# Performance work log

Measured on AMD Instinct MI355X. Metric: run time of the kernel, lower is better.

The kernel has to match this reference:

```python
import jax, jax.numpy as jnp
import numpy as np

B, C, H, W = 8, 21, 512, 512
MAX_M = 0.5   # args.ldam_max_m
S = 30.0      # args.ldam_s


def setup_inputs() -> dict:
    key = jax.random.key(0)
    k1, k2 = jax.random.split(key)
    pred = jax.random.normal(k1, (B, C, H, W), dtype=jnp.float32)
    target = jax.random.randint(k2, (B, H, W), 0, C, dtype=jnp.int32)  # class labels (argmax of one-hot)
    return {"pred": pred, "target": target}


def reference(pred, target):
    labels = target.reshape(-1)  # [N]
    # m_list: per-class pixel counts == sum of one-hot target over (0,2,3)
    counts = jnp.zeros((C,), dtype=pred.dtype).at[labels].add(1.0)
    m_list = 1.0 / jnp.sqrt(jnp.sqrt(counts + 1e-4))
    m_list = m_list * (MAX_M / jnp.max(m_list))

    logits = pred.transpose(0, 2, 3, 1).reshape(-1, C)  # [N, C]
    batch_m = m_list[labels]                            # gather == matmul(m_list, one_hot^T)
    onehot = jax.nn.one_hot(labels, C, dtype=logits.dtype)
    output = logits - batch_m[:, None] * onehot         # subtract margin only at target class

    logp = jax.nn.log_softmax(S * output, axis=-1)
    nll = -jnp.take_along_axis(logp, labels[:, None].astype(jnp.int32), axis=1)[:, 0]
    return jnp.mean(nll)
```

## Files before the change

kernel.cpp:

```cpp
#include <hip/hip_runtime.h>

static constexpr int   Cc  = 21;
static constexpr int   HWn = 512 * 512;
static constexpr int   Nn  = 8 * HWn;
static constexpr float MAXM  = 0.5f;
static constexpr float Sc    = 30.0f;
static constexpr float LOG2E = 1.4426950408889634f;
static constexpr float LN2   = 0.6931471805599453f;

static constexpr int WS_COUNTS = 0;
static constexpr int WS_ACC    = 96;
static constexpr int WS_SM     = 128;

__global__ __launch_bounds__(256) void hist_kernel(const int4* __restrict__ t4,
                                                   int* __restrict__ counts) {
    __shared__ int lh[Cc];
    int t = threadIdx.x;
    if (t < Cc) lh[t] = 0;
    __syncthreads();
    int tid = blockIdx.x * 256 + t;
    int4 v = t4[tid];
    atomicAdd(&lh[v.x], 1);
    atomicAdd(&lh[v.y], 1);
    atomicAdd(&lh[v.z], 1);
    atomicAdd(&lh[v.w], 1);
    __syncthreads();
    if (t < Cc) atomicAdd(&counts[t], lh[t]);
}

__global__ __launch_bounds__(64) void mlist_kernel(const int* __restrict__ counts,
                                                   float* __restrict__ sm2) {
    int t = threadIdx.x;
    float mval = 0.0f;
    if (t < Cc) {
        float cnt = (float)counts[t] + 1e-4f;
        mval = 1.0f / sqrtf(sqrtf(cnt));
    }
    float mx = mval;
    #pragma unroll
    for (int o = 32; o >= 1; o >>= 1) mx = fmaxf(mx, __shfl_down(mx, o));
    mx = __shfl(mx, 0);
    if (t < Cc) sm2[t] = Sc * LOG2E * mval * (MAXM / mx);
}

__global__ __launch_bounds__(256, 2) void loss_kernel(const float* __restrict__ pred,
                                                      const int4* __restrict__ t4,
                                                      const float* __restrict__ smg,
                                                      double* __restrict__ acc) {
    __shared__ float s_sm[Cc];
    __shared__ float wsum[4];
    int t = threadIdx.x;
    if (t < Cc) s_sm[t] = smg[t];
    __syncthreads();

    int tid = blockIdx.x * 256 + t;
    int n0  = tid * 4;
    int b   = n0 >> 18;
    int hw  = n0 & (HWn - 1);
    const float4* p4 = (const float4*)(pred + (size_t)b * Cc * HWn + hw);

    float4 x[Cc];
    #pragma unroll
    for (int c = 0; c < Cc; ++c) x[c] = p4[(size_t)c * (HWn / 4)];

    int4 y4 = t4[tid];
    int ys[4] = {y4.x, y4.y, y4.z, y4.w};
    float smy[4];
    #pragma unroll
    for (int k = 0; k < 4; ++k) smy[k] = s_sm[ys[k]];

    const float S2 = Sc * LOG2E;

    float mx[4] = {-1e30f, -1e30f, -1e30f, -1e30f};
    float vy[4] = {0.f, 0.f, 0.f, 0.f};
    #pragma unroll
    for (int c = 0; c < Cc; ++c) {
        float xs[4] = {x[c].x, x[c].y, x[c].z, x[c].w};
        #pragma unroll
        for (int k = 0; k < 4; ++k) {
            bool  isy = (c == ys[k]);
            float val = fmaf(S2, xs[k], isy ? -smy[k] : 0.0f);
            mx[k] = fmaxf(mx[k], val);
            vy[k] = isy ? val : vy[k];
        }
    }

    float nll2 = 0.0f;
    #pragma unroll
    for (int k = 0; k < 4; ++k) {
        float cb = -mx[k];
        float cy = -smy[k] - mx[k];
        float sum = 0.0f;
        #pragma unroll
        for (int c = 0; c < Cc; ++c) {
            float xs = (k == 0) ? x[c].x : (k == 1) ? x[c].y : (k == 2) ? x[c].z : x[c].w;
            sum += exp2f(fmaf(S2, xs, (c == ys[k]) ? cy : cb));
        }
        nll2 += __log2f(sum) + mx[k] - vy[k];
    }
    float nll = nll2 * LN2;

    #pragma unroll
    for (int o = 32; o >= 1; o >>= 1) nll += __shfl_down(nll, o);

    int wave = t >> 6;
    int lane = t & 63;
    if (lane == 0) wsum[wave] = nll;
    __syncthreads();
    if (t == 0) {
        float bsum = wsum[0] + wsum[1] + wsum[2] + wsum[3];
        atomicAdd(acc, (double)bsum);
    }
}

__global__ void final_kernel(const double* __restrict__ acc, float* __restrict__ out) {
    out[0] = (float)(acc[0] / (double)Nn);
}

extern "C" void kernel_launch(void* const* d_in, const int* in_sizes, int n_in,
                              void* d_out, int out_size, void* d_ws, size_t ws_size,
                              hipStream_t stream) {
    const float* pred   = (const float*)d_in[0];
    const int*   target = (const int*)d_in[1];
    float*       out    = (float*)d_out;

    char* ws = (char*)d_ws;
    int*    counts = (int*)(ws + WS_COUNTS);
    double* acc    = (double*)(ws + WS_ACC);
    float*  sm     = (float*)(ws + WS_SM);

    hipMemsetAsync(d_ws, 0, 256, stream);

    hist_kernel <<<Nn / 4 / 256, 256, 0, stream>>>((const int4*)target, counts);
    mlist_kernel<<<1,            64,  0, stream>>>(counts, sm);
    loss_kernel <<<Nn / 4 / 256, 256, 0, stream>>>(pred, (const int4*)target, sm, acc);
    final_kernel<<<1,            1,   0, stream>>>(acc, out);
}
```

Measured before the change: 272.4 us.

## Fold mlist and final kernels into last-block epilogues; halve hist blocks

Removes the single-block mlist and final kernels by having the last finishing block of the histogram kernel compute the margin list, and the last block of the loss kernel write the mean, using atomic done counters with thread fences. The histogram kernel now processes two int4 per thread with per-wave shared-memory sub-histograms to cut LDS atomic contention and halve the block count. This saves two kernel launches and their gaps, at the cost of extra global atomics and fences at the end of each block.

```diff
diff --git a/kernel.cpp b/kernel.cpp
--- a/kernel.cpp
+++ b/kernel.cpp
@@ -8,45 +8,66 @@
 static constexpr float LOG2E = 1.4426950408889634f;
 static constexpr float LN2   = 0.6931471805599453f;
 
-static constexpr int WS_COUNTS = 0;
-static constexpr int WS_ACC    = 96;
-static constexpr int WS_SM     = 128;
+static constexpr int WS_COUNTS    = 0;
+static constexpr int WS_HIST_DONE = 88;
+static constexpr int WS_LOSS_DONE = 92;
+static constexpr int WS_ACC       = 96;
+static constexpr int WS_SM        = 112;
 
 __global__ __launch_bounds__(256) void hist_kernel(const int4* __restrict__ t4,
-                                                   int* __restrict__ counts) {
-    __shared__ int lh[Cc];
-    int t = threadIdx.x;
-    if (t < Cc) lh[t] = 0;
+                                                   int* __restrict__ counts,
+                                                   int* __restrict__ hist_done,
+                                                   float* __restrict__ sm2) {
+    __shared__ int lh[4][Cc];
+    __shared__ int is_last;
+    int t    = threadIdx.x;
+    int wave = t >> 6;
+    if (t < Cc) { lh[0][t] = 0; lh[1][t] = 0; lh[2][t] = 0; lh[3][t] = 0; }
     __syncthreads();
+
     int tid = blockIdx.x * 256 + t;
-    int4 v = t4[tid];
-    atomicAdd(&lh[v.x], 1);
-    atomicAdd(&lh[v.y], 1);
-    atomicAdd(&lh[v.z], 1);
-    atomicAdd(&lh[v.w], 1);
+    int4 a = t4[tid];
+    int4 b = t4[tid + (Nn / 8)];
+    atomicAdd(&lh[wave][a.x], 1);
+    atomicAdd(&lh[wave][a.y], 1);
+    atomicAdd(&lh[wave][a.z], 1);
+    atomicAdd(&lh[wave][a.w], 1);
+    atomicAdd(&lh[wave][b.x], 1);
+    atomicAdd(&lh[wave][b.y], 1);
+    atomicAdd(&lh[wave][b.z], 1);
+    atomicAdd(&lh[wave][b.w], 1);
     __syncthreads();
-    if (t < Cc) atomicAdd(&counts[t], lh[t]);
-}
+    if (t < Cc) atomicAdd(&counts[t], lh[0][t] + lh[1][t] + lh[2][t] + lh[3][t]);
+    __syncthreads();
 
-__global__ __launch_bounds__(64) void mlist_kernel(const int* __restrict__ counts,
-                                                   float* __restrict__ sm2) {
-    int t = threadIdx.x;
-    float mval = 0.0f;
-    if (t < Cc) {
-        float cnt = (float)counts[t] + 1e-4f;
-        mval = 1.0f / sqrtf(sqrtf(cnt));
+    if (t == 0) {
+        __threadfence();
+        int prev = atomicAdd(hist_done, 1);
+        is_last = (prev == (int)gridDim.x - 1);
     }
-    float mx = mval;
-    #pragma unroll
-    for (int o = 32; o >= 1; o >>= 1) mx = fmaxf(mx, __shfl_down(mx, o));
-    mx = __shfl(mx, 0);
-    if (t < Cc) sm2[t] = Sc * LOG2E * mval * (MAXM / mx);
+    __syncthreads();
+
+    if (is_last && t < 64) {
+        __threadfence();
+        float mval = 0.0f;
+        if (t < Cc) {
+            int cnt = atomicAdd(&counts[t], 0);
+            mval = 1.0f / sqrtf(sqrtf((float)cnt + 1e-4f));
+        }
+        float mx = mval;
+        #pragma unroll
+        for (int o = 32; o >= 1; o >>= 1) mx = fmaxf(mx, __shfl_down(mx, o));
+        mx = __shfl(mx, 0);
+        if (t < Cc) sm2[t] = Sc * LOG2E * mval * (MAXM / mx);
+    }
 }
 
 __global__ __launch_bounds__(256, 2) void loss_kernel(const float* __restrict__ pred,
                                                       const int4* __restrict__ t4,
                                                       const float* __restrict__ smg,
-                                                      double* __restrict__ acc) {
+                                                      double* __restrict__ acc,
+                                                      int* __restrict__ loss_done,
+                                                      float* __restrict__ out) {
     __shared__ float s_sm[Cc];
     __shared__ float wsum[4];
     int t = threadIdx.x;
@@ -110,11 +131,14 @@
     if (t == 0) {
         float bsum = wsum[0] + wsum[1] + wsum[2] + wsum[3];
         atomicAdd(acc, (double)bsum);
+        __threadfence();
+        int prev = atomicAdd(loss_done, 1);
+        if (prev == (int)gridDim.x - 1) {
+            __threadfence();
+            double total = atomicAdd(acc, 0.0);
+            out[0] = (float)(total / (double)Nn);
+        }
     }
-}
-
-__global__ void final_kernel(const double* __restrict__ acc, float* __restrict__ out) {
-    out[0] = (float)(acc[0] / (double)Nn);
 }
 
 extern "C" void kernel_launch(void* const* d_in, const int* in_sizes, int n_in,
@@ -125,14 +149,16 @@
     float*       out    = (float*)d_out;
 
     char* ws = (char*)d_ws;
-    int*    counts = (int*)(ws + WS_COUNTS);
-    double* acc    = (double*)(ws + WS_ACC);
-    float*  sm     = (float*)(ws + WS_SM);
+    int*    counts    = (int*)(ws + WS_COUNTS);
+    int*    hist_done = (int*)(ws + WS_HIST_DONE);
+    int*    loss_done = (int*)(ws + WS_LOSS_DONE);
+    double* acc       = (double*)(ws + WS_ACC);
+    float*  sm        = (float*)(ws + WS_SM);
 
     hipMemsetAsync(d_ws, 0, 256, stream);
 
-    hist_kernel <<<Nn / 4 / 256, 256, 0, stream>>>((const int4*)target, counts);
-    mlist_kernel<<<1,            64,  0, stream>>>(counts, sm);
-    loss_kernel <<<Nn / 4 / 256, 256, 0, stream>>>(pred, (const int4*)target, sm, acc);
-    final_kernel<<<1,            1,   0, stream>>>(acc, out);
+    hist_kernel<<<Nn / 8 / 256, 256, 0, stream>>>((const int4*)target, counts,
+                                                  hist_done, sm);
+    loss_kernel<<<Nn / 4 / 256, 256, 0, stream>>>(pred, (const int4*)target, sm,
+                                                  acc, loss_done, out);
 }
```

After: 385.4 us. 1.41x slower.
